# Kernel optimization log

Measured on AMD Instinct MI355X. Metric: run time of the kernel, lower is better.

Reference implementation:

```python
import jax
import jax.numpy as jnp
import numpy as np

# ---- static config (matches init_kwargs) ----
V_PATCH_NUMS = [1, 2, 3, 4, 5, 6, 8, 10, 13, 16]
SN = len(V_PATCH_NUMS)
BETA = 0.25
RESI = 0.5          # Phi residual ratio
K_PHI = 4           # share_quant_resi -> PhiPartiallyShared with 4 convs
_ticks = np.linspace(1.0 / 3 / K_PHI, 1 - 1.0 / 3 / K_PHI, K_PHI)  # K==4 branch
PHI_IDX = [int(np.argmin(np.abs(_ticks - si / (SN - 1)))) for si in range(SN)]


def _area_matrix(n_in, n_out):
    """Row-stochastic matrix replicating F.interpolate(mode='area') == adaptive_avg_pool (1D)."""
    M = np.zeros((n_out, n_in), np.float32)
    for i in range(n_out):
        s = (i * n_in) // n_out
        e = -((-(i + 1) * n_in) // n_out)  # ceil
        M[i, s:e] = 1.0 / (e - s)
    return M


def _bicubic_matrix(n_in, n_out):
    """1D bicubic (a=-0.75, align_corners=False, border clamp), matching torch F.interpolate."""
    A = -0.75
    M = np.zeros((n_out, n_in), np.float32)
    scale = n_in / n_out
    for i in range(n_out):
        src = (i + 0.5) * scale - 0.5
        f = int(np.floor(src))
        t = src - f
        for k in range(4):           # taps at f-1 .. f+2
            j = f - 1 + k
            d = abs(src - j)
            if d <= 1.0:
                w = (A + 2) * d ** 3 - (A + 3) * d ** 2 + 1.0
            elif d < 2.0:
                w = A * d ** 3 - 5 * A * d ** 2 + 8 * A * d - 4 * A
            else:
                w = 0.0
            M[i, min(max(j, 0), n_in - 1)] += w
    return M


def _phi(h, w, b):
    # Phi: h*(1-r) + conv3x3(h)*r
    conv = jax.lax.conv_general_dilated(
        h, w, window_strides=(1, 1), padding='SAME',
        dimension_numbers=('NCHW', 'OIHW', 'NCHW')) + b[None, :, None, None]
    return h * (1.0 - RESI) + conv * RESI


def setup_inputs() -> dict:
    key = jax.random.key(0)
    k1, k2, k3 = jax.random.split(key, 3)
    B, C, H = 32, 32, 16
    V = 8192
    f_BChw = jax.random.normal(k1, (B, C, H, H), dtype=jnp.float32)
    emb = jax.random.normal(k2, (V, C), dtype=jnp.float32)
    conv_w = jax.random.normal(k3, (K_PHI, C, C, 3, 3), dtype=jnp.float32) * 0.05
    conv_b = jnp.zeros((K_PHI, C), dtype=jnp.float32)
    return {"f_BChw": f_BChw, "emb": emb, "conv_w": conv_w, "conv_b": conv_b}


def reference(f_BChw, emb, conv_w, conv_b):
    B, C, H, W = f_BChw.shape
    dt = f_BChw.dtype
    f_ng = jax.lax.stop_gradient(f_BChw)
    f_rest = f_ng
    f_hat = jnp.zeros_like(f_ng)
    emb_ng = jax.lax.stop_gradient(emb)     # distances use embedding.weight.data
    emb_sq = jnp.sum(emb_ng ** 2, axis=1)   # [V]
    loss = jnp.zeros((), dt)
    for si, pn in enumerate(V_PATCH_NUMS):
        r = jax.lax.stop_gradient(f_rest)
        if si != SN - 1:
            P = jnp.asarray(_area_matrix(H, pn), dt)
            z = jnp.einsum('ph,bchw,qw->bpqc', P, r, P)   # area pool -> [B,pn,pn,C]
        else:
            z = r.transpose(0, 2, 3, 1)
        z_NC = z.reshape(-1, C)
        d = jnp.sum(z_NC ** 2, axis=1, keepdims=True) + emb_sq - 2.0 * (z_NC @ emb_ng.T)
        idx = jnp.argmin(d, axis=1)                        # [B*pn*pn]
        h = jnp.take(emb, idx, axis=0).reshape(B, pn, pn, C).transpose(0, 3, 1, 2)
        if si != SN - 1:
            U = jnp.asarray(_bicubic_matrix(pn, H), dt)
            h = jnp.einsum('hp,bcpq,wq->bchw', U, h, U)    # bicubic upsample
        pi = PHI_IDX[si]
        h = _phi(h, conv_w[pi], conv_b[pi])
        f_hat = f_hat + h
        f_rest = f_rest - h
        loss = loss + BETA * jnp.mean((jax.lax.stop_gradient(f_hat) - f_BChw) ** 2) \
                    + jnp.mean((f_hat - f_ng) ** 2)
    loss = loss / SN
    f_hat_out = jax.lax.stop_gradient(f_hat) - f_ng + f_BChw   # straight-through
    return f_hat_out, loss
```

## Files before the change

### kernel.cpp

```cpp
#include <hip/hip_runtime.h>
#include <math.h>
#include <stdint.h>

#define B_ 32
#define C_ 32
#define H_ 16
#define V_ 8192
#define HW_ 256
#define NELEM (B_*C_*H_*H_)
#define TBYTES 6208
#define ZPL 262144

typedef short bf16x8 __attribute__((ext_vector_type(8)));
typedef unsigned short u16x8 __attribute__((ext_vector_type(8)));
typedef float f32x4 __attribute__((ext_vector_type(4)));
typedef unsigned long long ull;

__device__ __forceinline__ unsigned int fkey(float f) {
    unsigned int u = __float_as_uint(f);
    return (u & 0x80000000u) ? ~u : (u | 0x80000000u);
}
__device__ __forceinline__ unsigned short f2bf(float x) {
    unsigned int u = __float_as_uint(x);
    unsigned int r = u + 0x7fffu + ((u >> 16) & 1u);
    return (unsigned short)(r >> 16);
}
__device__ __forceinline__ float bf2f(unsigned short h) {
    return __uint_as_float(((unsigned int)h) << 16);
}

__global__ void __launch_bounds__(256) k_init(
    const float* __restrict__ f, const float* __restrict__ emb,
    float* __restrict__ f_rest, float* __restrict__ f_hat,
    char* __restrict__ blob, float* __restrict__ lossAcc)
{
    int i = blockIdx.x*256 + threadIdx.x;
    if (i < NELEM) { float v = f[i]; f_rest[i] = v; f_hat[i] = 0.f; }
    if (i < 512*64) {
        int t = i >> 6, l = i & 63;
        int row = t*16 + (l & 15);
        int k0 = (l >> 4) * 8;
        const float* er = emb + row*C_ + k0;
        u16x8 h0, h1, h2;
        #pragma unroll
        for (int j = 0; j < 8; ++j) {
            float x = -2.f * er[j];
            unsigned short b0 = f2bf(x);  float r1 = x - bf2f(b0);
            unsigned short b1 = f2bf(r1); float r2 = r1 - bf2f(b1);
            unsigned short b2 = f2bf(r2);
            h0[j] = b0; h1[j] = b1; h2[j] = b2;
        }
        char* tb = blob + (size_t)t*TBYTES;
        *(u16x8*)(tb +        l*16) = h0;
        *(u16x8*)(tb + 2048 + l*16) = h1;
        *(u16x8*)(tb + 4096 + l*16) = h2;
        if ((l >> 4) == 0) {
            const float4* e4 = (const float4*)(emb + row*C_);
            float s = 0.f;
            #pragma unroll
            for (int cc = 0; cc < 8; ++cc) {
                float4 ev = e4[cc];
                s += ev.x*ev.x + ev.y*ev.y + ev.z*ev.z + ev.w*ev.w;
            }
            *(float*)(tb + 6144 + (l & 15)*4) = s;
        }
    }
    if (i == 0) lossAcc[0] = 0.f;
}

__global__ void __launch_bounds__(256) k_pool(
    const float* __restrict__ f_rest, unsigned short* __restrict__ zb,
    ull* __restrict__ best, int pn, int N)
{
    int gid = blockIdx.x*256 + threadIdx.x;
    if (gid >= N*C_) return;
    int c = gid & 31;
    int n = gid >> 5;
    if (c == 0) best[n] = ~0ull;
    int pp = pn*pn;
    int b = n / pp;
    int rem = n - b*pp;
    int p = rem / pn;
    int q = rem - p*pn;
    int hs = (p*H_)/pn,  he = ((p+1)*H_ + pn-1)/pn;
    int ws = (q*H_)/pn,  we = ((q+1)*H_ + pn-1)/pn;
    const float* base = f_rest + ((size_t)(b*C_ + c))*HW_;
    float s = 0.f;
    for (int hh = hs; hh < he; ++hh)
        for (int ww = ws; ww < we; ++ww)
            s += base[hh*H_ + ww];
    float inv = (1.f/(float)(he-hs)) * (1.f/(float)(we-ws));
    float x = s * inv;
    unsigned short b0 = f2bf(x);  float r1 = x - bf2f(b0);
    unsigned short b1 = f2bf(r1); float r2 = r1 - bf2f(b1);
    unsigned short b2 = f2bf(r2);
    size_t o = (size_t)n*C_ + c;
    zb[o] = b0; zb[o + ZPL] = b1; zb[o + 2*ZPL] = b2;
}

__device__ __forceinline__ void qstep(
    const bf16x8 a0, const bf16x8 a1, const bf16x8 a2, const f32x4 e2v,
    const bf16x8* Bf, int cbase, float& dmin, int& imin)
{
    f32x4 acc = e2v;
    acc = __builtin_amdgcn_mfma_f32_16x16x32_bf16(a0, Bf[0], acc, 0, 0, 0);
    acc = __builtin_amdgcn_mfma_f32_16x16x32_bf16(a1, Bf[0], acc, 0, 0, 0);
    acc = __builtin_amdgcn_mfma_f32_16x16x32_bf16(a0, Bf[1], acc, 0, 0, 0);
    acc = __builtin_amdgcn_mfma_f32_16x16x32_bf16(a2, Bf[0], acc, 0, 0, 0);
    acc = __builtin_amdgcn_mfma_f32_16x16x32_bf16(a1, Bf[1], acc, 0, 0, 0);
    acc = __builtin_amdgcn_mfma_f32_16x16x32_bf16(a0, Bf[2], acc, 0, 0, 0);
    float mt = fminf(fminf(acc.x, acc.y), fminf(acc.z, acc.w));
    if (mt < dmin) {
        dmin = mt;
        imin = cbase + ((acc.x==mt) ? 0 : (acc.y==mt) ? 1 : (acc.z==mt) ? 2 : 3);
    }
}

__global__ void __launch_bounds__(256, 2) k_vqm(
    const char* __restrict__ blob, const unsigned short* __restrict__ zb,
    ull* __restrict__ best, int N, int lvs)
{
    int tid = threadIdx.x, lane = tid & 63, w = tid >> 6;
    int qtiles_total = N >> 4;
    int qb = blockIdx.x >> lvs;
    int vc = blockIdx.x & ((1 << lvs) - 1);
    int tiles = 512 >> lvs;
    int t0 = vc * tiles;
    int qt0 = qb*16 + w*4;
    int qr = lane & 15, kq = lane >> 4;

    bf16x8 Bf0[3], Bf1[3], Bf2[3], Bf3[3];
    int qv0, qv1, qv2, qv3;
    {
        int qtj;
        size_t o;
        qtj = qt0 + 0; qv0 = (qtj < qtiles_total);
        o = (size_t)((qv0 ? qtj : 0)*16 + qr)*C_ + kq*8;
        Bf0[0] = *(const bf16x8*)(zb + o);
        Bf0[1] = *(const bf16x8*)(zb + o + ZPL);
        Bf0[2] = *(const bf16x8*)(zb + o + 2*ZPL);
        qtj = qt0 + 1; qv1 = (qtj < qtiles_total);
        o = (size_t)((qv1 ? qtj : 0)*16 + qr)*C_ + kq*8;
        Bf1[0] = *(const bf16x8*)(zb + o);
        Bf1[1] = *(const bf16x8*)(zb + o + ZPL);
        Bf1[2] = *(const bf16x8*)(zb + o + 2*ZPL);
        qtj = qt0 + 2; qv2 = (qtj < qtiles_total);
        o = (size_t)((qv2 ? qtj : 0)*16 + qr)*C_ + kq*8;
        Bf2[0] = *(const bf16x8*)(zb + o);
        Bf2[1] = *(const bf16x8*)(zb + o + ZPL);
        Bf2[2] = *(const bf16x8*)(zb + o + 2*ZPL);
        qtj = qt0 + 3; qv3 = (qtj < qtiles_total);
        o = (size_t)((qv3 ? qtj : 0)*16 + qr)*C_ + kq*8;
        Bf3[0] = *(const bf16x8*)(zb + o);
        Bf3[1] = *(const bf16x8*)(zb + o + ZPL);
        Bf3[2] = *(const bf16x8*)(zb + o + 2*ZPL);
    }

    float dmin[4]; int imin[4];
    #pragma unroll
    for (int j = 0; j < 4; ++j) { dmin[j] = __builtin_inff(); imin[j] = 0; }

    const char* tb = blob + (size_t)t0*TBYTES;
    bf16x8 Xa0, Xa1, Xa2; f32x4 Xe;
    bf16x8 Ya0, Ya1, Ya2; f32x4 Ye;
    Xa0 = *(const bf16x8*)(tb +        lane*16);
    Xa1 = *(const bf16x8*)(tb + 2048 + lane*16);
    Xa2 = *(const bf16x8*)(tb + 4096 + lane*16);
    Xe  = *(const f32x4*)(tb + 6144 + kq*16);

    for (int tt = 0; tt < tiles; tt += 2) {
        const char* nb = tb + TBYTES;
        Ya0 = *(const bf16x8*)(nb +        lane*16);
        Ya1 = *(const bf16x8*)(nb + 2048 + lane*16);
        Ya2 = *(const bf16x8*)(nb + 4096 + lane*16);
        Ye  = *(const f32x4*)(nb + 6144 + kq*16);
        {
            int cbase = (t0 + tt)*16 + kq*4;
            qstep(Xa0, Xa1, Xa2, Xe, Bf0, cbase, dmin[0], imin[0]);
            qstep(Xa0, Xa1, Xa2, Xe, Bf1, cbase, dmin[1], imin[1]);
            qstep(Xa0, Xa1, Xa2, Xe, Bf2, cbase, dmin[2], imin[2]);
            qstep(Xa0, Xa1, Xa2, Xe, Bf3, cbase, dmin[3], imin[3]);
        }
        const char* nb2 = (tt + 2 < tiles) ? tb + 2*TBYTES : tb;
        Xa0 = *(const bf16x8*)(nb2 +        lane*16);
        Xa1 = *(const bf16x8*)(nb2 + 2048 + lane*16);
        Xa2 = *(const bf16x8*)(nb2 + 4096 + lane*16);
        Xe  = *(const f32x4*)(nb2 + 6144 + kq*16);
        {
            int cbase = (t0 + tt + 1)*16 + kq*4;
            qstep(Ya0, Ya1, Ya2, Ye, Bf0, cbase, dmin[0], imin[0]);
            qstep(Ya0, Ya1, Ya2, Ye, Bf1, cbase, dmin[1], imin[1]);
            qstep(Ya0, Ya1, Ya2, Ye, Bf2, cbase, dmin[2], imin[2]);
            qstep(Ya0, Ya1, Ya2, Ye, Bf3, cbase, dmin[3], imin[3]);
        }
        tb += 2*TBYTES;
    }

    int qvv[4] = {qv0, qv1, qv2, qv3};
    #pragma unroll
    for (int j = 0; j < 4; ++j) {
        ull key = ((ull)fkey(dmin[j]) << 32) | (unsigned int)imin[j];
        ull o1 = __shfl_xor(key, 16); key = o1 < key ? o1 : key;
        ull o2 = __shfl_xor(key, 32); key = o2 < key ? o2 : key;
        if (kq == 0 && qvv[j]) {
            int q = (qt0 + j)*16 + qr;
            atomicMin(best + q, key);
        }
    }
}

__device__ __forceinline__ void cubic_taps(int i, int pn, float* wt, int* col) {
    double src = ((double)i + 0.5) * ((double)pn / 16.0) - 0.5;
    double fl = floor(src);
    const double A = -0.75;
    #pragma unroll
    for (int k = 0; k < 4; ++k) {
        double j = fl - 1.0 + (double)k;
        double d = fabs(src - j);
        double w;
        if (d <= 1.0)      w = ((A+2.0)*d - (A+3.0))*d*d + 1.0;
        else if (d < 2.0)  w = ((A*d - 5.0*A)*d + 8.0*A)*d - 4.0*A;
        else               w = 0.0;
        wt[k] = (float)w;
        int jj = (int)j;
        col[k] = jj < 0 ? 0 : (jj > pn-1 ? pn-1 : jj);
    }
}

__global__ void __launch_bounds__(256) k_upphi(
    const ull* __restrict__ best,
    const float* __restrict__ emb,
    const float* __restrict__ cw, const float* __restrict__ cb,
    const float* __restrict__ forig,
    float* __restrict__ f_hat, float* __restrict__ f_rest,
    float* __restrict__ lossAcc, int pn,
    int pn2, unsigned short* __restrict__ zb, ull* __restrict__ bestN)
{
    __shared__ float hup[16][16][33];
    __shared__ float red[4];
    int bi = blockIdx.x >> 3;
    int g  = blockIdx.x & 7;
    int tid = threadIdx.x;
    int h = tid >> 4, w = tid & 15;

    float wh[4]; int th[4];
    float wwt[4]; int tw[4];
    cubic_taps(h, pn, wh, th);
    cubic_taps(w, pn, wwt, tw);

    float acc[32];
    #pragma unroll
    for (int c = 0; c < 32; ++c) acc[c] = 0.f;
    const ull* bptr = best + bi*pn*pn;
    for (int i = 0; i < 4; ++i) {
        if (wh[i] == 0.f) continue;
        for (int j = 0; j < 4; ++j) {
            float wt = wh[i]*wwt[j];
            if (wt == 0.f) continue;
            unsigned int idx = (unsigned int)(bptr[th[i]*pn + tw[j]] & 0xffffffffull);
            const float4* e4 = (const float4*)(emb + (size_t)idx*C_);
            #pragma unroll
            for (int cc = 0; cc < 8; ++cc) {
                float4 ev = e4[cc];
                acc[cc*4+0] = fmaf(wt, ev.x, acc[cc*4+0]);
                acc[cc*4+1] = fmaf(wt, ev.y, acc[cc*4+1]);
                acc[cc*4+2] = fmaf(wt, ev.z, acc[cc*4+2]);
                acc[cc*4+3] = fmaf(wt, ev.w, acc[cc*4+3]);
            }
        }
    }
    #pragma unroll
    for (int c = 0; c < 32; ++c) hup[h][w][c] = acc[c];
    __syncthreads();

    int co0 = g*4;
    float o4[4];
    #pragma unroll
    for (int k = 0; k < 4; ++k) o4[k] = cb[co0+k];
    for (int ci = 0; ci < 32; ++ci) {
        float hv[9];
        #pragma unroll
        for (int dh = 0; dh < 3; ++dh) {
            int hh = h + dh - 1;
            #pragma unroll
            for (int dw = 0; dw < 3; ++dw) {
                int ww2 = w + dw - 1;
                bool ok = (hh >= 0) & (hh < 16) & (ww2 >= 0) & (ww2 < 16);
                hv[dh*3+dw] = ok ? hup[hh & 15][ww2 & 15][ci] : 0.f;
            }
        }
        #pragma unroll
        for (int k = 0; k < 4; ++k) {
            const float* wr = cw + ((size_t)(co0+k)*C_ + ci)*9;
            float s = 0.f;
            #pragma unroll
            for (int p2 = 0; p2 < 9; ++p2) s = fmaf(hv[p2], wr[p2], s);
            o4[k] += s;
        }
    }
    __syncthreads();

    float sq = 0.f;
    #pragma unroll
    for (int k = 0; k < 4; ++k) {
        float hv0 = hup[h][w][co0+k];
        float outv = 0.5f*hv0 + 0.5f*o4[k];
        size_t off = ((size_t)(bi*C_ + co0 + k))*HW_ + h*16 + w;
        float fh = f_hat[off] + outv;
        f_hat[off] = fh;
        float fr = f_rest[off] - outv;
        f_rest[off] = fr;
        hup[h][w][co0+k] = fr;
        float df = fh - forig[off];
        sq = fmaf(df, df, sq);
    }
    #pragma unroll
    for (int o2 = 32; o2 > 0; o2 >>= 1) sq += __shfl_down(sq, o2, 64);
    if ((tid & 63) == 0) red[tid >> 6] = sq;
    __syncthreads();
    if (tid == 0) atomicAdd(lossAcc, (red[0]+red[1])+(red[2]+red[3]));

    if (pn2 > 0 && h < pn2 && w < pn2) {
        int hs = (h*H_)/pn2,  he2 = ((h+1)*H_ + pn2-1)/pn2;
        int ws2 = (w*H_)/pn2, we2 = ((w+1)*H_ + pn2-1)/pn2;
        float inv = (1.f/(float)(he2-hs)) * (1.f/(float)(we2-ws2));
        int n = bi*pn2*pn2 + h*pn2 + w;
        #pragma unroll
        for (int k = 0; k < 4; ++k) {
            float s = 0.f;
            for (int hh = hs; hh < he2; ++hh)
                for (int ww = ws2; ww < we2; ++ww)
                    s += hup[hh][ww][co0+k];
            float x = s * inv;
            unsigned short b0 = f2bf(x);  float r1 = x - bf2f(b0);
            unsigned short b1 = f2bf(r1); float r2 = r1 - bf2f(b1);
            unsigned short b2 = f2bf(r2);
            size_t o = (size_t)n*C_ + co0 + k;
            zb[o] = b0; zb[o + ZPL] = b1; zb[o + 2*ZPL] = b2;
        }
        if (g == 0) bestN[n] = ~0ull;
    }
}

__global__ void __launch_bounds__(256) k_final(
    const float* __restrict__ f_hat, const float* __restrict__ lossAcc,
    float* __restrict__ out)
{
    int i = blockIdx.x*256 + threadIdx.x;
    if (i < NELEM) out[i] = f_hat[i];
    if (i == 0) out[NELEM] = lossAcc[0] * 1.25f / ((float)NELEM * 10.f);
}

extern "C" void kernel_launch(void* const* d_in, const int* in_sizes, int n_in,
                              void* d_out, int out_size, void* d_ws, size_t ws_size,
                              hipStream_t stream)
{
    const float* f   = (const float*)d_in[0];
    const float* emb = (const float*)d_in[1];
    const float* cw  = (const float*)d_in[2];
    const float* cb  = (const float*)d_in[3];
    float* out = (float*)d_out;
    char* ws = (char*)d_ws;
    ull*   best0  = (ull*)ws;
    ull*   best1  = (ull*)(ws + 65536);
    float* f_rest = (float*)(ws + 131072);
    float* f_hat  = (float*)(ws + 131072 + 1048576);
    unsigned short* zb = (unsigned short*)(ws + 2228224);
    char*  blob   = ws + 3801088;
    float* lossAcc = (float*)(ws + 6979584);

    volatile double a   = 1.0/3.0/4.0;
    volatile double bb  = 1.0 - a;
    volatile double stp = (bb - a) / 3.0;
    double ticks[4];
    for (int i = 0; i < 4; ++i) { volatile double m = (double)i * stp; ticks[i] = m + a; }
    ticks[3] = bb;
    static const int pns[10] = {1,2,3,4,5,6,8,10,13,16};
    int phi_idx[10];
    for (int si = 0; si < 10; ++si) {
        volatile double x = (double)si / 9.0;
        int bi = 0; double bd = fabs(ticks[0] - x);
        for (int k = 1; k < 4; ++k) {
            double d = fabs(ticks[k] - x);
            if (d < bd) { bd = d; bi = k; }
        }
        phi_idx[si] = bi;
    }

    k_init<<<1024, 256, 0, stream>>>(f, emb, f_rest, f_hat, blob, lossAcc);
    k_pool<<<4, 256, 0, stream>>>(f_rest, zb, best0, 1, 32);

    static const int lvss[10] = {6,6,6,6,6,6,6,5,5,4};
    for (int si = 0; si < 10; ++si) {
        int pn = pns[si];
        int N = B_*pn*pn;
        int qtiles = N >> 4;
        int qblocks = (qtiles + 15)/16;
        int lvs = lvss[si];
        ull* bcur  = (si & 1) ? best1 : best0;
        ull* bnext = (si & 1) ? best0 : best1;
        k_vqm<<<qblocks << lvs, 256, 0, stream>>>(blob, zb, bcur, N, lvs);
        const float* cwp = cw + (size_t)phi_idx[si]*C_*C_*9;
        const float* cbp = cb + (size_t)phi_idx[si]*C_;
        int pn2 = (si < 9) ? pns[si+1] : 0;
        k_upphi<<<B_*8, 256, 0, stream>>>(bcur, emb, cwp, cbp, f, f_hat, f_rest,
                                          lossAcc, pn, pn2, zb, bnext);
    }
    k_final<<<1024, 256, 0, stream>>>(f_hat, lossAcc, out);
}
```

Baseline: 437.1 us.

## Split bicubic upsample into separate kernel to avoid redundant per-block recomputation

Moves the bicubic upsampling of the selected codebook vectors out of the fused upsample+conv kernel into a new per-element kernel that writes the upsampled map to a workspace buffer. The conv kernel then loads this buffer into shared memory instead of recomputing the upsample in each of the 8 output-channel-group blocks per batch. This removes 8x redundant gather and FMA work, but adds an extra kernel launch per scale and a global-memory round trip of the upsampled tensor.

Result: no change. 444.6 us (+1.7%).

```diff
diff --git a/kernel.cpp b/kernel.cpp
--- a/kernel.cpp
+++ b/kernel.cpp
@@ -227,13 +227,41 @@
     }
 }
 
-__global__ void __launch_bounds__(256) k_upphi(
-    const ull* __restrict__ best,
-    const float* __restrict__ emb,
+__global__ void __launch_bounds__(256) k_up(
+    const ull* __restrict__ best, const float* __restrict__ emb,
+    float* __restrict__ h_up, int pn)
+{
+    int i = blockIdx.x*256 + threadIdx.x;
+    int c  = i & 31;
+    int px = (i >> 5) & 255;
+    int bi = i >> 13;
+    int h = px >> 4, w = px & 15;
+    float wh[4]; int th[4];
+    float wwt[4]; int tw[4];
+    cubic_taps(h, pn, wh, th);
+    cubic_taps(w, pn, wwt, tw);
+    const ull* bptr = best + bi*pn*pn;
+    float acc = 0.f;
+    #pragma unroll
+    for (int ii = 0; ii < 4; ++ii) {
+        if (wh[ii] == 0.f) continue;
+        #pragma unroll
+        for (int j = 0; j < 4; ++j) {
+            float wt = wh[ii]*wwt[j];
+            if (wt == 0.f) continue;
+            unsigned int idx = (unsigned int)(bptr[th[ii]*pn + tw[j]] & 0xffffffffull);
+            acc = fmaf(wt, emb[(size_t)idx*C_ + c], acc);
+        }
+    }
+    h_up[(size_t)bi*8192 + px*32 + c] = acc;
+}
+
+__global__ void __launch_bounds__(256) k_conv(
+    const float* __restrict__ h_up,
     const float* __restrict__ cw, const float* __restrict__ cb,
     const float* __restrict__ forig,
     float* __restrict__ f_hat, float* __restrict__ f_rest,
-    float* __restrict__ lossAcc, int pn,
+    float* __restrict__ lossAcc,
     int pn2, unsigned short* __restrict__ zb, ull* __restrict__ bestN)
 {
     __shared__ float hup[16][16][33];
@@ -243,34 +271,17 @@
     int tid = threadIdx.x;
     int h = tid >> 4, w = tid & 15;
 
-    float wh[4]; int th[4];
-    float wwt[4]; int tw[4];
-    cubic_taps(h, pn, wh, th);
-    cubic_taps(w, pn, wwt, tw);
-
-    float acc[32];
-    #pragma unroll
-    for (int c = 0; c < 32; ++c) acc[c] = 0.f;
-    const ull* bptr = best + bi*pn*pn;
-    for (int i = 0; i < 4; ++i) {
-        if (wh[i] == 0.f) continue;
-        for (int j = 0; j < 4; ++j) {
-            float wt = wh[i]*wwt[j];
-            if (wt == 0.f) continue;
-            unsigned int idx = (unsigned int)(bptr[th[i]*pn + tw[j]] & 0xffffffffull);
-            const float4* e4 = (const float4*)(emb + (size_t)idx*C_);
-            #pragma unroll
-            for (int cc = 0; cc < 8; ++cc) {
-                float4 ev = e4[cc];
-                acc[cc*4+0] = fmaf(wt, ev.x, acc[cc*4+0]);
-                acc[cc*4+1] = fmaf(wt, ev.y, acc[cc*4+1]);
-                acc[cc*4+2] = fmaf(wt, ev.z, acc[cc*4+2]);
-                acc[cc*4+3] = fmaf(wt, ev.w, acc[cc*4+3]);
-            }
-        }
-    }
-    #pragma unroll
-    for (int c = 0; c < 32; ++c) hup[h][w][c] = acc[c];
+    const float4* src = (const float4*)(h_up + (size_t)bi*8192);
+    #pragma unroll
+    for (int cc = 0; cc < 8; ++cc) {
+        int f4 = cc*256 + tid;
+        float4 v = src[f4];
+        int px = f4 >> 3, c0 = (f4 & 7)*4;
+        hup[px >> 4][px & 15][c0+0] = v.x;
+        hup[px >> 4][px & 15][c0+1] = v.y;
+        hup[px >> 4][px & 15][c0+2] = v.z;
+        hup[px >> 4][px & 15][c0+3] = v.w;
+    }
     __syncthreads();
 
     int co0 = g*4;
@@ -368,6 +379,7 @@
     unsigned short* zb = (unsigned short*)(ws + 2228224);
     char*  blob   = ws + 3801088;
     float* lossAcc = (float*)(ws + 6979584);
+    float* h_up   = (float*)(ws + 7340032);
 
     volatile double a   = 1.0/3.0/4.0;
     volatile double bb  = 1.0 - a;
@@ -400,11 +412,12 @@
         ull* bcur  = (si & 1) ? best1 : best0;
         ull* bnext = (si & 1) ? best0 : best1;
         k_vqm<<<qblocks << lvs, 256, 0, stream>>>(blob, zb, bcur, N, lvs);
+        k_up<<<1024, 256, 0, stream>>>(bcur, emb, h_up, pn);
         const float* cwp = cw + (size_t)phi_idx[si]*C_*C_*9;
         const float* cbp = cb + (size_t)phi_idx[si]*C_;
         int pn2 = (si < 9) ? pns[si+1] : 0;
-        k_upphi<<<B_*8, 256, 0, stream>>>(bcur, emb, cwp, cbp, f, f_hat, f_rest,
-                                          lossAcc, pn, pn2, zb, bnext);
+        k_conv<<<B_*8, 256, 0, stream>>>(h_up, cwp, cbp, f, f_hat, f_rest,
+                                         lossAcc, pn2, zb, bnext);
     }
     k_final<<<1024, 256, 0, stream>>>(f_hat, lossAcc, out);
 }
```

## Fuse all VQ scales into one cooperative persistent kernel with per-image barriers

Applied to the files above, without the earlier changes.

Replaces the per-scale k_pool/k_vqm/k_upphi launch chain with a single cooperative kernel. Eight blocks handle each image, keeping f_rest and f_hat for their four channels in shared memory and syncing through per-image atomic counter barriers. This removes about twenty kernel launches and the global round-trips of f_rest/f_hat between scales. In exchange, the codebook search is split into fixed 8-way chunks per image rather than tuned per scale, and correctness depends on spin-wait barriers with all 256 blocks co-resident.

Result: slower. 868.5 us (+98.7%).

```diff
diff --git a/kernel.cpp b/kernel.cpp
--- a/kernel.cpp
+++ b/kernel.cpp
@@ -6,7 +6,6 @@
 #define C_ 32
 #define H_ 16
 #define V_ 8192
-#define HW_ 256
 #define NELEM (B_*C_*H_*H_)
 #define TBYTES 6208
 #define ZPL 262144
@@ -30,72 +29,39 @@
 }
 
 __global__ void __launch_bounds__(256) k_init(
-    const float* __restrict__ f, const float* __restrict__ emb,
-    float* __restrict__ f_rest, float* __restrict__ f_hat,
-    char* __restrict__ blob, float* __restrict__ lossAcc)
+    const float* __restrict__ emb, char* __restrict__ blob,
+    float* __restrict__ lossAcc, unsigned int* __restrict__ ctr)
 {
     int i = blockIdx.x*256 + threadIdx.x;
-    if (i < NELEM) { float v = f[i]; f_rest[i] = v; f_hat[i] = 0.f; }
-    if (i < 512*64) {
-        int t = i >> 6, l = i & 63;
-        int row = t*16 + (l & 15);
-        int k0 = (l >> 4) * 8;
-        const float* er = emb + row*C_ + k0;
-        u16x8 h0, h1, h2;
+    int t = i >> 6, l = i & 63;
+    int row = t*16 + (l & 15);
+    int k0 = (l >> 4) * 8;
+    const float* er = emb + row*C_ + k0;
+    u16x8 h0, h1, h2;
+    #pragma unroll
+    for (int j = 0; j < 8; ++j) {
+        float x = -2.f * er[j];
+        unsigned short b0 = f2bf(x);  float r1 = x - bf2f(b0);
+        unsigned short b1 = f2bf(r1); float r2 = r1 - bf2f(b1);
+        unsigned short b2 = f2bf(r2);
+        h0[j] = b0; h1[j] = b1; h2[j] = b2;
+    }
+    char* tb = blob + (size_t)t*TBYTES;
+    *(u16x8*)(tb +        l*16) = h0;
+    *(u16x8*)(tb + 2048 + l*16) = h1;
+    *(u16x8*)(tb + 4096 + l*16) = h2;
+    if ((l >> 4) == 0) {
+        const float4* e4 = (const float4*)(emb + row*C_);
+        float s = 0.f;
         #pragma unroll
-        for (int j = 0; j < 8; ++j) {
-            float x = -2.f * er[j];
-            unsigned short b0 = f2bf(x);  float r1 = x - bf2f(b0);
-            unsigned short b1 = f2bf(r1); float r2 = r1 - bf2f(b1);
-            unsigned short b2 = f2bf(r2);
-            h0[j] = b0; h1[j] = b1; h2[j] = b2;
-        }
-        char* tb = blob + (size_t)t*TBYTES;
-        *(u16x8*)(tb +        l*16) = h0;
-        *(u16x8*)(tb + 2048 + l*16) = h1;
-        *(u16x8*)(tb + 4096 + l*16) = h2;
-        if ((l >> 4) == 0) {
-            const float4* e4 = (const float4*)(emb + row*C_);
-            float s = 0.f;
-            #pragma unroll
-            for (int cc = 0; cc < 8; ++cc) {
-                float4 ev = e4[cc];
-                s += ev.x*ev.x + ev.y*ev.y + ev.z*ev.z + ev.w*ev.w;
-            }
-            *(float*)(tb + 6144 + (l & 15)*4) = s;
-        }
-    }
+        for (int cc = 0; cc < 8; ++cc) {
+            float4 ev = e4[cc];
+            s += ev.x*ev.x + ev.y*ev.y + ev.z*ev.z + ev.w*ev.w;
+        }
+        *(float*)(tb + 6144 + (l & 15)*4) = s;
+    }
+    if (i < 1024) ctr[i] = 0;
     if (i == 0) lossAcc[0] = 0.f;
-}
-
-__global__ void __launch_bounds__(256) k_pool(
-    const float* __restrict__ f_rest, unsigned short* __restrict__ zb,
-    ull* __restrict__ best, int pn, int N)
-{
-    int gid = blockIdx.x*256 + threadIdx.x;
-    if (gid >= N*C_) return;
-    int c = gid & 31;
-    int n = gid >> 5;
-    if (c == 0) best[n] = ~0ull;
-    int pp = pn*pn;
-    int b = n / pp;
-    int rem = n - b*pp;
-    int p = rem / pn;
-    int q = rem - p*pn;
-    int hs = (p*H_)/pn,  he = ((p+1)*H_ + pn-1)/pn;
-    int ws = (q*H_)/pn,  we = ((q+1)*H_ + pn-1)/pn;
-    const float* base = f_rest + ((size_t)(b*C_ + c))*HW_;
-    float s = 0.f;
-    for (int hh = hs; hh < he; ++hh)
-        for (int ww = ws; ww < we; ++ww)
-            s += base[hh*H_ + ww];
-    float inv = (1.f/(float)(he-hs)) * (1.f/(float)(we-ws));
-    float x = s * inv;
-    unsigned short b0 = f2bf(x);  float r1 = x - bf2f(b0);
-    unsigned short b1 = f2bf(r1); float r2 = r1 - bf2f(b1);
-    unsigned short b2 = f2bf(r2);
-    size_t o = (size_t)n*C_ + c;
-    zb[o] = b0; zb[o + ZPL] = b1; zb[o + 2*ZPL] = b2;
 }
 
 __device__ __forceinline__ void qstep(
@@ -113,99 +79,6 @@
     if (mt < dmin) {
         dmin = mt;
         imin = cbase + ((acc.x==mt) ? 0 : (acc.y==mt) ? 1 : (acc.z==mt) ? 2 : 3);
-    }
-}
-
-__global__ void __launch_bounds__(256, 2) k_vqm(
-    const char* __restrict__ blob, const unsigned short* __restrict__ zb,
-    ull* __restrict__ best, int N, int lvs)
-{
-    int tid = threadIdx.x, lane = tid & 63, w = tid >> 6;
-    int qtiles_total = N >> 4;
-    int qb = blockIdx.x >> lvs;
-    int vc = blockIdx.x & ((1 << lvs) - 1);
-    int tiles = 512 >> lvs;
-    int t0 = vc * tiles;
-    int qt0 = qb*16 + w*4;
-    int qr = lane & 15, kq = lane >> 4;
-
-    bf16x8 Bf0[3], Bf1[3], Bf2[3], Bf3[3];
-    int qv0, qv1, qv2, qv3;
-    {
-        int qtj;
-        size_t o;
-        qtj = qt0 + 0; qv0 = (qtj < qtiles_total);
-        o = (size_t)((qv0 ? qtj : 0)*16 + qr)*C_ + kq*8;
-        Bf0[0] = *(const bf16x8*)(zb + o);
-        Bf0[1] = *(const bf16x8*)(zb + o + ZPL);
-        Bf0[2] = *(const bf16x8*)(zb + o + 2*ZPL);
-        qtj = qt0 + 1; qv1 = (qtj < qtiles_total);
-        o = (size_t)((qv1 ? qtj : 0)*16 + qr)*C_ + kq*8;
-        Bf1[0] = *(const bf16x8*)(zb + o);
-        Bf1[1] = *(const bf16x8*)(zb + o + ZPL);
-        Bf1[2] = *(const bf16x8*)(zb + o + 2*ZPL);
-        qtj = qt0 + 2; qv2 = (qtj < qtiles_total);
-        o = (size_t)((qv2 ? qtj : 0)*16 + qr)*C_ + kq*8;
-        Bf2[0] = *(const bf16x8*)(zb + o);
-        Bf2[1] = *(const bf16x8*)(zb + o + ZPL);
-        Bf2[2] = *(const bf16x8*)(zb + o + 2*ZPL);
-        qtj = qt0 + 3; qv3 = (qtj < qtiles_total);
-        o = (size_t)((qv3 ? qtj : 0)*16 + qr)*C_ + kq*8;
-        Bf3[0] = *(const bf16x8*)(zb + o);
-        Bf3[1] = *(const bf16x8*)(zb + o + ZPL);
-        Bf3[2] = *(const bf16x8*)(zb + o + 2*ZPL);
-    }
-
-    float dmin[4]; int imin[4];
-    #pragma unroll
-    for (int j = 0; j < 4; ++j) { dmin[j] = __builtin_inff(); imin[j] = 0; }
-
-    const char* tb = blob + (size_t)t0*TBYTES;
-    bf16x8 Xa0, Xa1, Xa2; f32x4 Xe;
-    bf16x8 Ya0, Ya1, Ya2; f32x4 Ye;
-    Xa0 = *(const bf16x8*)(tb +        lane*16);
-    Xa1 = *(const bf16x8*)(tb + 2048 + lane*16);
-    Xa2 = *(const bf16x8*)(tb + 4096 + lane*16);
-    Xe  = *(const f32x4*)(tb + 6144 + kq*16);
-
-    for (int tt = 0; tt < tiles; tt += 2) {
-        const char* nb = tb + TBYTES;
-        Ya0 = *(const bf16x8*)(nb +        lane*16);
-        Ya1 = *(const bf16x8*)(nb + 2048 + lane*16);
-        Ya2 = *(const bf16x8*)(nb + 4096 + lane*16);
-        Ye  = *(const f32x4*)(nb + 6144 + kq*16);
-        {
-            int cbase = (t0 + tt)*16 + kq*4;
-            qstep(Xa0, Xa1, Xa2, Xe, Bf0, cbase, dmin[0], imin[0]);
-            qstep(Xa0, Xa1, Xa2, Xe, Bf1, cbase, dmin[1], imin[1]);
-            qstep(Xa0, Xa1, Xa2, Xe, Bf2, cbase, dmin[2], imin[2]);
-            qstep(Xa0, Xa1, Xa2, Xe, Bf3, cbase, dmin[3], imin[3]);
-        }
-        const char* nb2 = (tt + 2 < tiles) ? tb + 2*TBYTES : tb;
-        Xa0 = *(const bf16x8*)(nb2 +        lane*16);
-        Xa1 = *(const bf16x8*)(nb2 + 2048 + lane*16);
-        Xa2 = *(const bf16x8*)(nb2 + 4096 + lane*16);
-        Xe  = *(const f32x4*)(nb2 + 6144 + kq*16);
-        {
-            int cbase = (t0 + tt + 1)*16 + kq*4;
-            qstep(Ya0, Ya1, Ya2, Ye, Bf0, cbase, dmin[0], imin[0]);
-            qstep(Ya0, Ya1, Ya2, Ye, Bf1, cbase, dmin[1], imin[1]);
-            qstep(Ya0, Ya1, Ya2, Ye, Bf2, cbase, dmin[2], imin[2]);
-            qstep(Ya0, Ya1, Ya2, Ye, Bf3, cbase, dmin[3], imin[3]);
-        }
-        tb += 2*TBYTES;
-    }
-
-    int qvv[4] = {qv0, qv1, qv2, qv3};
-    #pragma unroll
-    for (int j = 0; j < 4; ++j) {
-        ull key = ((ull)fkey(dmin[j]) << 32) | (unsigned int)imin[j];
-        ull o1 = __shfl_xor(key, 16); key = o1 < key ? o1 : key;
-        ull o2 = __shfl_xor(key, 32); key = o2 < key ? o2 : key;
-        if (kq == 0 && qvv[j]) {
-            int q = (qt0 + j)*16 + qr;
-            atomicMin(best + q, key);
-        }
     }
 }
 
@@ -227,147 +100,292 @@
     }
 }
 
-__global__ void __launch_bounds__(256) k_upphi(
-    const ull* __restrict__ best,
-    const float* __restrict__ emb,
-    const float* __restrict__ cw, const float* __restrict__ cb,
-    const float* __restrict__ forig,
-    float* __restrict__ f_hat, float* __restrict__ f_rest,
-    float* __restrict__ lossAcc, int pn,
-    int pn2, unsigned short* __restrict__ zb, ull* __restrict__ bestN)
-{
-    __shared__ float hup[16][16][33];
-    __shared__ float red[4];
-    int bi = blockIdx.x >> 3;
-    int g  = blockIdx.x & 7;
-    int tid = threadIdx.x;
-    int h = tid >> 4, w = tid & 15;
-
-    float wh[4]; int th[4];
-    float wwt[4]; int tw[4];
-    cubic_taps(h, pn, wh, th);
-    cubic_taps(w, pn, wwt, tw);
-
-    float acc[32];
-    #pragma unroll
-    for (int c = 0; c < 32; ++c) acc[c] = 0.f;
-    const ull* bptr = best + bi*pn*pn;
-    for (int i = 0; i < 4; ++i) {
-        if (wh[i] == 0.f) continue;
-        for (int j = 0; j < 4; ++j) {
-            float wt = wh[i]*wwt[j];
-            if (wt == 0.f) continue;
-            unsigned int idx = (unsigned int)(bptr[th[i]*pn + tw[j]] & 0xffffffffull);
-            const float4* e4 = (const float4*)(emb + (size_t)idx*C_);
+__device__ __forceinline__ void img_barrier(unsigned int* c) {
+    __syncthreads();
+    if (threadIdx.x == 0) {
+        __hip_atomic_fetch_add(c, 1u, __ATOMIC_RELEASE, __HIP_MEMORY_SCOPE_AGENT);
+        while (__hip_atomic_load(c, __ATOMIC_ACQUIRE, __HIP_MEMORY_SCOPE_AGENT) < 8u)
+            __builtin_amdgcn_s_sleep(1);
+    }
+    __syncthreads();
+}
+
+__device__ __forceinline__ void pool_to_zb(
+    const float* frL, unsigned short* zb, int bi, int pn2, int co0, int tid)
+{
+    int pp2 = pn2*pn2;
+    int items = pp2*4;
+    for (int it = tid; it < items; it += 512) {
+        int k = it & 3, cell = it >> 2;
+        int h2 = cell / pn2, w2 = cell - h2*pn2;
+        int hs = (h2*H_)/pn2,  he = ((h2+1)*H_ + pn2-1)/pn2;
+        int ws = (w2*H_)/pn2,  we = ((w2+1)*H_ + pn2-1)/pn2;
+        float s = 0.f;
+        for (int hh = hs; hh < he; ++hh)
+            for (int ww = ws; ww < we; ++ww)
+                s += frL[(hh*H_+ww)*4 + k];
+        float inv = (1.f/(float)(he-hs)) * (1.f/(float)(we-ws));
+        float x = s * inv;
+        unsigned short b0 = f2bf(x);  float r1 = x - bf2f(b0);
+        unsigned short b1 = f2bf(r1); float r2 = r1 - bf2f(b1);
+        unsigned short b2 = f2bf(r2);
+        size_t o = (size_t)(bi*pp2 + cell)*C_ + co0 + k;
+        zb[o] = b0; zb[o + ZPL] = b1; zb[o + 2*ZPL] = b2;
+    }
+}
+
+struct MegaP {
+    const float *f, *emb, *cw, *cb;
+    const char* blob;
+    unsigned short* zb;
+    ull* best0; ull* best1;
+    unsigned int* ctr;
+    float* lossAcc; float* out;
+    int phi[10];
+};
+
+__global__ void __launch_bounds__(512, 2) k_mega(MegaP P)
+{
+    __shared__ float huL[256*33];
+    __shared__ float frL[256*4];
+    __shared__ float fhL[256*4];
+    __shared__ float wtT[64];
+    __shared__ int   colT[64];
+    __shared__ float red[8];
+
+    const int tid = threadIdx.x;
+    const int bi = blockIdx.x >> 3;
+    const int j  = blockIdx.x & 7;
+    const int co0 = j*4;
+    const int lane = tid & 63, wid = tid >> 6;
+    const int qr = lane & 15, kq = lane >> 4;
+    const float* fimg = P.f + (size_t)bi*8192;
+
+    for (int it = tid; it < 1024; it += 512) {
+        int k = it >> 8, px = it & 255;
+        frL[px*4 + k] = fimg[(co0+k)*256 + px];
+        fhL[px*4 + k] = 0.f;
+    }
+    if (tid < 256) P.best0[bi*256 + tid] = ~0ull;
+    __syncthreads();
+    pool_to_zb(frL, P.zb, bi, 1, co0, tid);
+    img_barrier(&P.ctr[bi*32 + 0]);
+
+    static const int pns[10] = {1,2,3,4,5,6,8,10,13,16};
+
+    for (int si = 0; si < 10; ++si) {
+        const int pn = pns[si], pp = pn*pn;
+        const int qtiles = (pp + 15) >> 4;
+        const int ngroups = (qtiles + 3) >> 2;
+        ull* bcur  = (si & 1) ? P.best1 : P.best0;
+        ull* bnext = (si & 1) ? P.best0 : P.best1;
+
+        {
+            const int t0 = j*64 + wid*8;
+            const unsigned short* zq = P.zb + (size_t)bi*pp*C_;
+            for (int g = 0; g < ngroups; ++g) {
+                bf16x8 B0[3], B1[3], B2[3], B3[3];
+                int v0, v1, v2, v3;
+                {
+                    int row; size_t o;
+                    row = (g*4+0)*16 + qr; v0 = (row < pp);
+                    o = (size_t)(v0 ? row : 0)*C_ + kq*8;
+                    B0[0] = *(const bf16x8*)(zq + o);
+                    B0[1] = *(const bf16x8*)(zq + o + ZPL);
+                    B0[2] = *(const bf16x8*)(zq + o + 2*ZPL);
+                    row = (g*4+1)*16 + qr; v1 = (row < pp);
+                    o = (size_t)(v1 ? row : 0)*C_ + kq*8;
+                    B1[0] = *(const bf16x8*)(zq + o);
+                    B1[1] = *(const bf16x8*)(zq + o + ZPL);
+                    B1[2] = *(const bf16x8*)(zq + o + 2*ZPL);
+                    row = (g*4+2)*16 + qr; v2 = (row < pp);
+                    o = (size_t)(v2 ? row : 0)*C_ + kq*8;
+                    B2[0] = *(const bf16x8*)(zq + o);
+                    B2[1] = *(const bf16x8*)(zq + o + ZPL);
+                    B2[2] = *(const bf16x8*)(zq + o + 2*ZPL);
+                    row = (g*4+3)*16 + qr; v3 = (row < pp);
+                    o = (size_t)(v3 ? row : 0)*C_ + kq*8;
+                    B3[0] = *(const bf16x8*)(zq + o);
+                    B3[1] = *(const bf16x8*)(zq + o + ZPL);
+                    B3[2] = *(const bf16x8*)(zq + o + 2*ZPL);
+                }
+                float dmin[4]; int imin[4];
+                #pragma unroll
+                for (int q = 0; q < 4; ++q) { dmin[q] = __builtin_inff(); imin[q] = 0; }
+
+                const char* tb = P.blob + (size_t)t0*TBYTES;
+                bf16x8 Xa0, Xa1, Xa2; f32x4 Xe;
+                bf16x8 Ya0, Ya1, Ya2; f32x4 Ye;
+                Xa0 = *(const bf16x8*)(tb +        lane*16);
+                Xa1 = *(const bf16x8*)(tb + 2048 + lane*16);
+                Xa2 = *(const bf16x8*)(tb + 4096 + lane*16);
+                Xe  = *(const f32x4*)(tb + 6144 + kq*16);
+
+                for (int tt = 0; tt < 8; tt += 2) {
+                    const char* nb = tb + TBYTES;
+                    Ya0 = *(const bf16x8*)(nb +        lane*16);
+                    Ya1 = *(const bf16x8*)(nb + 2048 + lane*16);
+                    Ya2 = *(const bf16x8*)(nb + 4096 + lane*16);
+                    Ye  = *(const f32x4*)(nb + 6144 + kq*16);
+                    {
+                        int cbase = (t0 + tt)*16 + kq*4;
+                        qstep(Xa0, Xa1, Xa2, Xe, B0, cbase, dmin[0], imin[0]);
+                        qstep(Xa0, Xa1, Xa2, Xe, B1, cbase, dmin[1], imin[1]);
+                        qstep(Xa0, Xa1, Xa2, Xe, B2, cbase, dmin[2], imin[2]);
+                        qstep(Xa0, Xa1, Xa2, Xe, B3, cbase, dmin[3], imin[3]);
+                    }
+                    const char* nb2 = (tt + 2 < 8) ? tb + 2*TBYTES : tb;
+                    Xa0 = *(const bf16x8*)(nb2 +        lane*16);
+                    Xa1 = *(const bf16x8*)(nb2 + 2048 + lane*16);
+                    Xa2 = *(const bf16x8*)(nb2 + 4096 + lane*16);
+                    Xe  = *(const f32x4*)(nb2 + 6144 + kq*16);
+                    {
+                        int cbase = (t0 + tt + 1)*16 + kq*4;
+                        qstep(Ya0, Ya1, Ya2, Ye, B0, cbase, dmin[0], imin[0]);
+                        qstep(Ya0, Ya1, Ya2, Ye, B1, cbase, dmin[1], imin[1]);
+                        qstep(Ya0, Ya1, Ya2, Ye, B2, cbase, dmin[2], imin[2]);
+                        qstep(Ya0, Ya1, Ya2, Ye, B3, cbase, dmin[3], imin[3]);
+                    }
+                    tb += 2*TBYTES;
+                }
+                int vv[4] = {v0, v1, v2, v3};
+                #pragma unroll
+                for (int q = 0; q < 4; ++q) {
+                    ull key = ((ull)fkey(dmin[q]) << 32) | (unsigned int)imin[q];
+                    ull o1 = __shfl_xor(key, 16); key = o1 < key ? o1 : key;
+                    ull o2 = __shfl_xor(key, 32); key = o2 < key ? o2 : key;
+                    if (kq == 0 && vv[q])
+                        atomicMin(&bcur[bi*256 + (g*4+q)*16 + qr], key);
+                }
+            }
+        }
+        img_barrier(&P.ctr[bi*32 + 1 + 2*si]);
+
+        if (tid < 16) cubic_taps(tid, pn, &wtT[tid*4], &colT[tid*4]);
+        __syncthreads();
+
+        {
+            const ull* bptr = bcur + bi*256;
+            for (int it = tid; it < 8192; it += 512) {
+                int c = it & 31, px = it >> 5;
+                int h = px >> 4, w2 = px & 15;
+                float acc = 0.f;
+                #pragma unroll
+                for (int ii = 0; ii < 4; ++ii) {
+                    float whv = wtT[h*4+ii];
+                    if (whv == 0.f) continue;
+                    int th = colT[h*4+ii];
+                    #pragma unroll
+                    for (int jj = 0; jj < 4; ++jj) {
+                        float wt = whv * wtT[w2*4+jj];
+                        if (wt == 0.f) continue;
+                        unsigned int idx =
+                            (unsigned int)(bptr[th*pn + colT[w2*4+jj]] & 0xffffffffull);
+                        acc = fmaf(wt, P.emb[(size_t)idx*C_ + c], acc);
+                    }
+                }
+                huL[px*33 + c] = acc;
+            }
+        }
+        __syncthreads();
+
+        {
+            int px = tid & 255, half = tid >> 8;
+            int h = px >> 4, w2 = px & 15;
+            int cA = co0 + half*2;
+            const float* cwp = P.cw + (size_t)P.phi[si]*9216;
+            const float* cbp = P.cb + (size_t)P.phi[si]*C_;
+            float o0 = cbp[cA], o1 = cbp[cA+1];
+            for (int ci = 0; ci < 32; ++ci) {
+                float hv[9];
+                #pragma unroll
+                for (int dh = 0; dh < 3; ++dh) {
+                    int hh = h + dh - 1;
+                    #pragma unroll
+                    for (int dw = 0; dw < 3; ++dw) {
+                        int ww = w2 + dw - 1;
+                        bool ok = (hh >= 0) & (hh < 16) & (ww >= 0) & (ww < 16);
+                        int npx = ((hh & 15) << 4) | (ww & 15);
+                        hv[dh*3+dw] = ok ? huL[npx*33 + ci] : 0.f;
+                    }
+                }
+                const float* w0 = cwp + (size_t)cA*288 + ci*9;
+                const float* w1 = w0 + 288;
+                float s0 = 0.f, s1 = 0.f;
+                #pragma unroll
+                for (int t = 0; t < 9; ++t) {
+                    s0 = fmaf(hv[t], w0[t], s0);
+                    s1 = fmaf(hv[t], w1[t], s1);
+                }
+                o0 += s0; o1 += s1;
+            }
+            float sq = 0.f;
+            {
+                int co = cA, kk = half*2;
+                float hv0 = huL[px*33 + co];
+                float outv = 0.5f*hv0 + 0.5f*o0;
+                float fh = fhL[px*4 + kk] + outv;
+                fhL[px*4 + kk] = fh;
+                frL[px*4 + kk] -= outv;
+                float df = fh - fimg[co*256 + px];
+                sq = fmaf(df, df, sq);
+            }
+            {
+                int co = cA+1, kk = half*2+1;
+                float hv0 = huL[px*33 + co];
+                float outv = 0.5f*hv0 + 0.5f*o1;
+                float fh = fhL[px*4 + kk] + outv;
+                fhL[px*4 + kk] = fh;
+                frL[px*4 + kk] -= outv;
+                float df = fh - fimg[co*256 + px];
+                sq = fmaf(df, df, sq);
+            }
             #pragma unroll
-            for (int cc = 0; cc < 8; ++cc) {
-                float4 ev = e4[cc];
-                acc[cc*4+0] = fmaf(wt, ev.x, acc[cc*4+0]);
-                acc[cc*4+1] = fmaf(wt, ev.y, acc[cc*4+1]);
-                acc[cc*4+2] = fmaf(wt, ev.z, acc[cc*4+2]);
-                acc[cc*4+3] = fmaf(wt, ev.w, acc[cc*4+3]);
-            }
-        }
-    }
-    #pragma unroll
-    for (int c = 0; c < 32; ++c) hup[h][w][c] = acc[c];
-    __syncthreads();
-
-    int co0 = g*4;
-    float o4[4];
-    #pragma unroll
-    for (int k = 0; k < 4; ++k) o4[k] = cb[co0+k];
-    for (int ci = 0; ci < 32; ++ci) {
-        float hv[9];
-        #pragma unroll
-        for (int dh = 0; dh < 3; ++dh) {
-            int hh = h + dh - 1;
-            #pragma unroll
-            for (int dw = 0; dw < 3; ++dw) {
-                int ww2 = w + dw - 1;
-                bool ok = (hh >= 0) & (hh < 16) & (ww2 >= 0) & (ww2 < 16);
-                hv[dh*3+dw] = ok ? hup[hh & 15][ww2 & 15][ci] : 0.f;
-            }
-        }
-        #pragma unroll
-        for (int k = 0; k < 4; ++k) {
-            const float* wr = cw + ((size_t)(co0+k)*C_ + ci)*9;
+            for (int o2 = 32; o2 > 0; o2 >>= 1) sq += __shfl_down(sq, o2, 64);
+            if (lane == 0) red[wid] = sq;
+        }
+        __syncthreads();
+        if (tid == 0) {
             float s = 0.f;
             #pragma unroll
-            for (int p2 = 0; p2 < 9; ++p2) s = fmaf(hv[p2], wr[p2], s);
-            o4[k] += s;
-        }
-    }
-    __syncthreads();
-
-    float sq = 0.f;
-    #pragma unroll
-    for (int k = 0; k < 4; ++k) {
-        float hv0 = hup[h][w][co0+k];
-        float outv = 0.5f*hv0 + 0.5f*o4[k];
-        size_t off = ((size_t)(bi*C_ + co0 + k))*HW_ + h*16 + w;
-        float fh = f_hat[off] + outv;
-        f_hat[off] = fh;
-        float fr = f_rest[off] - outv;
-        f_rest[off] = fr;
-        hup[h][w][co0+k] = fr;
-        float df = fh - forig[off];
-        sq = fmaf(df, df, sq);
-    }
-    #pragma unroll
-    for (int o2 = 32; o2 > 0; o2 >>= 1) sq += __shfl_down(sq, o2, 64);
-    if ((tid & 63) == 0) red[tid >> 6] = sq;
-    __syncthreads();
-    if (tid == 0) atomicAdd(lossAcc, (red[0]+red[1])+(red[2]+red[3]));
-
-    if (pn2 > 0 && h < pn2 && w < pn2) {
-        int hs = (h*H_)/pn2,  he2 = ((h+1)*H_ + pn2-1)/pn2;
-        int ws2 = (w*H_)/pn2, we2 = ((w+1)*H_ + pn2-1)/pn2;
-        float inv = (1.f/(float)(he2-hs)) * (1.f/(float)(we2-ws2));
-        int n = bi*pn2*pn2 + h*pn2 + w;
-        #pragma unroll
-        for (int k = 0; k < 4; ++k) {
-            float s = 0.f;
-            for (int hh = hs; hh < he2; ++hh)
-                for (int ww = ws2; ww < we2; ++ww)
-                    s += hup[hh][ww][co0+k];
-            float x = s * inv;
-            unsigned short b0 = f2bf(x);  float r1 = x - bf2f(b0);
-            unsigned short b1 = f2bf(r1); float r2 = r1 - bf2f(b1);
-            unsigned short b2 = f2bf(r2);
-            size_t o = (size_t)n*C_ + co0 + k;
-            zb[o] = b0; zb[o + ZPL] = b1; zb[o + 2*ZPL] = b2;
-        }
-        if (g == 0) bestN[n] = ~0ull;
-    }
-}
-
-__global__ void __launch_bounds__(256) k_final(
-    const float* __restrict__ f_hat, const float* __restrict__ lossAcc,
-    float* __restrict__ out)
-{
-    int i = blockIdx.x*256 + threadIdx.x;
-    if (i < NELEM) out[i] = f_hat[i];
-    if (i == 0) out[NELEM] = lossAcc[0] * 1.25f / ((float)NELEM * 10.f);
+            for (int r = 0; r < 8; ++r) s += red[r];
+            atomicAdd(P.lossAcc, s);
+        }
+
+        if (si < 9) pool_to_zb(frL, P.zb, bi, pns[si+1], co0, tid);
+        if (tid < 256) bnext[bi*256 + tid] = ~0ull;
+        img_barrier(&P.ctr[bi*32 + 2 + 2*si]);
+    }
+
+    for (int it = tid; it < 1024; it += 512) {
+        int k = it >> 8, px = it & 255;
+        P.out[(size_t)bi*8192 + (co0+k)*256 + px] = fhL[px*4 + k];
+    }
+}
+
+__global__ void k_final(const float* __restrict__ lossAcc, float* __restrict__ out)
+{
+    if (blockIdx.x == 0 && threadIdx.x == 0)
+        out[NELEM] = lossAcc[0] * 1.25f / ((float)NELEM * 10.f);
 }
 
 extern "C" void kernel_launch(void* const* d_in, const int* in_sizes, int n_in,
                               void* d_out, int out_size, void* d_ws, size_t ws_size,
                               hipStream_t stream)
 {
-    const float* f   = (const float*)d_in[0];
-    const float* emb = (const float*)d_in[1];
-    const float* cw  = (const float*)d_in[2];
-    const float* cb  = (const float*)d_in[3];
-    float* out = (float*)d_out;
     char* ws = (char*)d_ws;
-    ull*   best0  = (ull*)ws;
-    ull*   best1  = (ull*)(ws + 65536);
-    float* f_rest = (float*)(ws + 131072);
-    float* f_hat  = (float*)(ws + 131072 + 1048576);
-    unsigned short* zb = (unsigned short*)(ws + 2228224);
-    char*  blob   = ws + 3801088;
-    float* lossAcc = (float*)(ws + 6979584);
+    MegaP P;
+    P.f   = (const float*)d_in[0];
+    P.emb = (const float*)d_in[1];
+    P.cw  = (const float*)d_in[2];
+    P.cb  = (const float*)d_in[3];
+    P.blob = ws;
+    P.zb   = (unsigned short*)(ws + 3178496);
+    P.best0 = (ull*)(ws + 4751360);
+    P.best1 = (ull*)(ws + 4816896);
+    P.ctr   = (unsigned int*)(ws + 4882432);
+    P.lossAcc = (float*)(ws + 4886528);
+    P.out = (float*)d_out;
 
     volatile double a   = 1.0/3.0/4.0;
     volatile double bb  = 1.0 - a;
@@ -375,36 +393,21 @@
     double ticks[4];
     for (int i = 0; i < 4; ++i) { volatile double m = (double)i * stp; ticks[i] = m + a; }
     ticks[3] = bb;
-    static const int pns[10] = {1,2,3,4,5,6,8,10,13,16};
-    int phi_idx[10];
     for (int si = 0; si < 10; ++si) {
         volatile double x = (double)si / 9.0;
-        int bi = 0; double bd = fabs(ticks[0] - x);
+        int bidx = 0; double bd = fabs(ticks[0] - x);
         for (int k = 1; k < 4; ++k) {
             double d = fabs(ticks[k] - x);
-            if (d < bd) { bd = d; bi = k; }
-        }
-        phi_idx[si] = bi;
-    }
-
-    k_init<<<1024, 256, 0, stream>>>(f, emb, f_rest, f_hat, blob, lossAcc);
-    k_pool<<<4, 256, 0, stream>>>(f_rest, zb, best0, 1, 32);
-
-    static const int lvss[10] = {6,6,6,6,6,6,6,5,5,4};
-    for (int si = 0; si < 10; ++si) {
-        int pn = pns[si];
-        int N = B_*pn*pn;
-        int qtiles = N >> 4;
-        int qblocks = (qtiles + 15)/16;
-        int lvs = lvss[si];
-        ull* bcur  = (si & 1) ? best1 : best0;
-        ull* bnext = (si & 1) ? best0 : best1;
-        k_vqm<<<qblocks << lvs, 256, 0, stream>>>(blob, zb, bcur, N, lvs);
-        const float* cwp = cw + (size_t)phi_idx[si]*C_*C_*9;
-        const float* cbp = cb + (size_t)phi_idx[si]*C_;
-        int pn2 = (si < 9) ? pns[si+1] : 0;
-        k_upphi<<<B_*8, 256, 0, stream>>>(bcur, emb, cwp, cbp, f, f_hat, f_rest,
-                                          lossAcc, pn, pn2, zb, bnext);
-    }
-    k_final<<<1024, 256, 0, stream>>>(f_hat, lossAcc, out);
-}
+            if (d < bd) { bd = d; bidx = k; }
+        }
+        P.phi[si] = bidx;
+    }
+
+    k_init<<<128, 256, 0, stream>>>(P.emb, (char*)ws, P.lossAcc, P.ctr);
+
+    void* args[] = { (void*)&P };
+    hipLaunchCooperativeKernel((const void*)k_mega, dim3(256), dim3(512),
+                               args, 0, stream);
+
+    k_final<<<1, 64, 0, stream>>>(P.lossAcc, P.out);
+}
```
